# Optimization experiments

Measured on AMD Instinct MI355X. Metric: run time of the kernel, lower is better.

The kernel has to match this reference:

```python
import jax, jax.numpy as jnp
import numpy as np

N_NODES = 100000
N_EDGES = 1600000
IN_C, HID_C, OUT_C = 128, 128, 64


def setup_inputs() -> dict:
    key = jax.random.key(0)
    ks = jax.random.split(key, 6)
    x = jax.random.normal(ks[0], (N_NODES, IN_C), dtype=jnp.float32)
    edge_index = jax.random.randint(ks[1], (2, N_EDGES), 0, N_NODES)
    W1 = jax.random.normal(ks[2], (IN_C, HID_C), dtype=jnp.float32) * (1.0 / np.sqrt(IN_C))
    b1 = jnp.zeros((HID_C,), dtype=jnp.float32)
    W2 = jax.random.normal(ks[3], (HID_C, OUT_C), dtype=jnp.float32) * (1.0 / np.sqrt(HID_C))
    b2 = jnp.zeros((OUT_C,), dtype=jnp.float32)
    return {"x": x, "edge_index": edge_index, "W1": W1, "b1": b1, "W2": W2, "b2": b2}


def gcn_conv(x, W, b, src, dst):
    # PyG GCNConv: D^{-1/2} (A + I) D^{-1/2} X W + b, with self-loops handled
    # analytically (no explicit self-loop edges materialized).
    h = x @ W                                             # [N, d_out]
    ones = jnp.ones(src.shape[0], dtype=h.dtype)
    deg = jax.ops.segment_sum(ones, dst, num_segments=N_NODES) + 1.0  # +1 self-loop
    dinv = jax.lax.rsqrt(deg)                             # deg >= 1, safe
    norm = dinv[src] * dinv[dst]                          # [E]
    msg = h[src] * norm[:, None]                          # gather + scale  [E, d_out]
    agg = jax.ops.segment_sum(msg, dst, num_segments=N_NODES)
    agg = agg + h * (dinv * dinv)[:, None]                # self-loop contribution
    return agg + b


def reference(x, edge_index, W1, b1, W2, b2):
    src, dst = edge_index[0], edge_index[1]
    h = jax.nn.relu(gcn_conv(x, W1, b1, src, dst))
    # dropout is identity in eval mode
    out = gcn_conv(h, W2, b2, src, dst)
    return out
```

## Files before the change

### kernel.cpp

```cpp
#include <hip/hip_runtime.h>

#define N_NODESC 100000
#define N_EDGESC 1600000
#define NB_BUCKETS 391
#define BUCKET_CAP 5120
#define CHUNK_A 4096

typedef __attribute__((ext_vector_type(4))) float floatx4;
typedef __attribute__((ext_vector_type(8))) short shortx8;

__device__ __forceinline__ unsigned short f32_to_bf16_rne(float f) {
    unsigned int u = __float_as_uint(f);
    unsigned int r = u + 0x7fffu + ((u >> 16) & 1u);
    return (unsigned short)(r >> 16);
}
__device__ __forceinline__ float bf16_to_f32(unsigned short h) {
    return __uint_as_float(((unsigned int)h) << 16);
}
__device__ __forceinline__ float bflo(unsigned int u) { return __uint_as_float(u << 16); }
__device__ __forceinline__ float bfhi(unsigned int u) { return __uint_as_float(u & 0xffff0000u); }
__device__ __forceinline__ unsigned int pack2bf(float a, float b) {
    return ((unsigned int)f32_to_bf16_rne(b) << 16) | (unsigned int)f32_to_bf16_rne(a);
}

__global__ __launch_bounds__(256) void k_wfrag_all(const float* __restrict__ W1,
        const float* __restrict__ W2,
        unsigned short* __restrict__ w1hi, unsigned short* __restrict__ w1lo,
        unsigned short* __restrict__ w2hi, unsigned short* __restrict__ w2lo,
        int* __restrict__ gcur) {
    int t = threadIdx.x;
    if (blockIdx.x == 0)
        for (int i = t; i < NB_BUCKETS; i += 256) gcur[i] = i * BUCKET_CAP;
    int idx = blockIdx.x * 256 + t;
    float f;
    int k, col, C, o;
    unsigned short *phi, *plo;
    if (idx < 16384) {
        k = idx >> 7; col = idx & 127; C = 8;
        f = W1[idx]; phi = w1hi; plo = w1lo;
    } else {
        int idx2 = idx - 16384;
        k = idx2 >> 6; col = idx2 & 63; C = 4;
        f = W2[idx2]; phi = w2hi; plo = w2lo;
    }
    unsigned short hi = f32_to_bf16_rne(f);
    unsigned short lo = f32_to_bf16_rne(f - bf16_to_f32(hi));
    int kc = k >> 5, q = (k >> 3) & 3, j = k & 7;
    int c = col >> 4, n = col & 15;
    o = (((kc * C + c) * 4 + q) * 16 + n) * 8 + j;
    phi[o] = hi; plo[o] = lo;
}

__global__ __launch_bounds__(1024) void k_bucket(const int* __restrict__ src,
        const int* __restrict__ dst, int* __restrict__ gcur,
        unsigned int* __restrict__ tmp) {
    __shared__ int hist[NB_BUCKETS];
    int t = threadIdx.x;
    for (int i = t; i < NB_BUCKETS; i += 1024) hist[i] = 0;
    __syncthreads();
    int base = blockIdx.x * CHUNK_A;
    int end = min(base + CHUNK_A, N_EDGESC);
    for (int e = base + t; e < end; e += 1024)
        atomicAdd(&hist[dst[e] >> 8], 1);
    __syncthreads();
    for (int i = t; i < NB_BUCKETS; i += 1024) {
        int c = hist[i];
        hist[i] = (c > 0) ? atomicAdd(&gcur[i], c) : 0;
    }
    __syncthreads();
    for (int e = base + t; e < end; e += 1024) {
        int d = dst[e];
        int pos = atomicAdd(&hist[d >> 8], 1);
        tmp[pos] = ((unsigned int)src[e] << 8) | (unsigned int)(d & 255);
    }
}

__global__ __launch_bounds__(1024) void k_place(const unsigned int* __restrict__ tmp,
        const int* __restrict__ gcur,
        int* __restrict__ swsrc, int* __restrict__ deg,
        int* __restrict__ row_ptr, float* __restrict__ dinv) {
    __shared__ int hist[256], scan[256], lcur[256];
    int b = blockIdx.x, t = threadIdx.x;
    int start = b * BUCKET_CAP;
    int end = gcur[b];
    if (t < 256) hist[t] = 0;
    __syncthreads();
    for (int i = start + t; i < end; i += 1024)
        atomicAdd(&hist[tmp[i] & 255u], 1);
    __syncthreads();
    int own = (t < 256) ? hist[t] : 0;
    if (t < 256) scan[t] = own;
    __syncthreads();
    for (int off = 1; off < 256; off <<= 1) {
        int add = (t >= off && t < 256) ? scan[t - off] : 0;
        __syncthreads();
        if (t < 256) scan[t] += add;
        __syncthreads();
    }
    if (t < 256) {
        int rp = start + scan[t] - own;
        lcur[t] = rp;
        int node = (b << 8) + t;
        if (node < N_NODESC) {
            deg[node] = own;
            row_ptr[node] = rp;
            dinv[node] = rsqrtf((float)own + 1.0f);
        }
    }
    __syncthreads();
    for (int i = start + t; i < end; i += 1024) {
        unsigned int v = tmp[i];
        int pos = atomicAdd(&lcur[v & 255u], 1);
        swsrc[pos] = (int)(v >> 8);
    }
}

template<int NOUT, int AFP32>
__global__ __launch_bounds__(256) void k_gemm_mfma(const void* __restrict__ Xv,
        const unsigned short* __restrict__ whi, const unsigned short* __restrict__ wlo,
        const float* __restrict__ dinv, unsigned short* __restrict__ H) {
    constexpr int C = NOUT / 16;
    constexpr int PITCH = NOUT + 4;
    __shared__ __align__(16) float etile[4][16][PITCH];
    int wv = threadIdx.x >> 6, lane = threadIdx.x & 63;
    int n16 = lane & 15, q = lane >> 4;
    int rowBase = blockIdx.x * 128 + wv * 32;
    floatx4 acc[2][C];
#pragma unroll
    for (int m = 0; m < 2; ++m)
#pragma unroll
        for (int c = 0; c < C; ++c) acc[m][c] = (floatx4){0.f, 0.f, 0.f, 0.f};

    const shortx8* whi8 = (const shortx8*)whi;
    const shortx8* wlo8 = (const shortx8*)wlo;

    for (int kc = 0; kc < 4; ++kc) {
        shortx8 ahi[2], alo[2];
#pragma unroll
        for (int m = 0; m < 2; ++m) {
            int r = rowBase + m * 16 + n16;
            if (r >= N_NODESC) r = N_NODESC - 1;
            if (AFP32) {
                const float* xp = &((const float*)Xv)[(size_t)r * 128 + kc * 32 + q * 8];
                floatx4 x0 = *(const floatx4*)xp;
                floatx4 x1 = *(const floatx4*)(xp + 4);
#pragma unroll
                for (int jj = 0; jj < 4; ++jj) {
                    unsigned short h0 = f32_to_bf16_rne(x0[jj]);
                    ahi[m][jj] = (short)h0;
                    alo[m][jj] = (short)f32_to_bf16_rne(x0[jj] - bf16_to_f32(h0));
                    unsigned short h1 = f32_to_bf16_rne(x1[jj]);
                    ahi[m][jj + 4] = (short)h1;
                    alo[m][jj + 4] = (short)f32_to_bf16_rne(x1[jj] - bf16_to_f32(h1));
                }
            } else {
                const unsigned short* xp = &((const unsigned short*)Xv)[(size_t)r * 128 + kc * 32 + q * 8];
                ahi[m] = *(const shortx8*)xp;
            }
        }
#pragma unroll
        for (int c = 0; c < C; ++c) {
            int fo = (kc * C + c) * 64 + lane;
            shortx8 bhi = whi8[fo];
            shortx8 blo = wlo8[fo];
#pragma unroll
            for (int m = 0; m < 2; ++m) {
                acc[m][c] = __builtin_amdgcn_mfma_f32_16x16x32_bf16(ahi[m], bhi, acc[m][c], 0, 0, 0);
                if (AFP32)
                    acc[m][c] = __builtin_amdgcn_mfma_f32_16x16x32_bf16(alo[m], bhi, acc[m][c], 0, 0, 0);
                acc[m][c] = __builtin_amdgcn_mfma_f32_16x16x32_bf16(ahi[m], blo, acc[m][c], 0, 0, 0);
            }
        }
    }
    constexpr int CPL = NOUT / 4;
#pragma unroll
    for (int m = 0; m < 2; ++m) {
        __syncthreads();
#pragma unroll
        for (int c = 0; c < C; ++c)
#pragma unroll
            for (int reg = 0; reg < 4; ++reg)
                etile[wv][q * 4 + reg][c * 16 + n16] = acc[m][c][reg];
        __syncthreads();
        int row = lane >> 2, cb = lane & 3;
        int r = rowBase + m * 16 + row;
        if (r < N_NODESC) {
            float dv = dinv[r];
            unsigned int po[CPL / 2];
#pragma unroll
            for (int i = 0; i < CPL / 4; ++i) {
                floatx4 v = *(const floatx4*)&etile[wv][row][cb * CPL + i * 4];
                po[i * 2 + 0] = pack2bf(v[0] * dv, v[1] * dv);
                po[i * 2 + 1] = pack2bf(v[2] * dv, v[3] * dv);
            }
            unsigned int* op = (unsigned int*)&H[(size_t)r * NOUT + cb * CPL];
#pragma unroll
            for (int i = 0; i < CPL / 8; ++i)
                *(uint4*)(op + i * 4) = *(uint4*)&po[i * 4];
        }
    }
}

__global__ __launch_bounds__(256) void k_agg128(const unsigned short* __restrict__ Hb,
        const int* __restrict__ swsrc, const int* __restrict__ row_ptr,
        const int* __restrict__ deg, const float* __restrict__ dinv,
        const float* __restrict__ bias, unsigned short* __restrict__ outb) {
    int node = blockIdx.x * 4 + (threadIdx.x >> 6);
    int lane = threadIdx.x & 63;
    int g = lane >> 4, l16 = lane & 15;
    int start = row_ptr[node];
    int end = start + deg[node];
    float acc[8] = {0.f, 0.f, 0.f, 0.f, 0.f, 0.f, 0.f, 0.f};
    int j = start + g;
    for (; j + 4 < end; j += 8) {
        int s0 = swsrc[j];
        int s1 = swsrc[j + 4];
        uint4 v0 = *(const uint4*)(Hb + (size_t)s0 * 128 + l16 * 8);
        uint4 v1 = *(const uint4*)(Hb + (size_t)s1 * 128 + l16 * 8);
        acc[0] += bflo(v0.x) + bflo(v1.x);
        acc[1] += bfhi(v0.x) + bfhi(v1.x);
        acc[2] += bflo(v0.y) + bflo(v1.y);
        acc[3] += bfhi(v0.y) + bfhi(v1.y);
        acc[4] += bflo(v0.z) + bflo(v1.z);
        acc[5] += bfhi(v0.z) + bfhi(v1.z);
        acc[6] += bflo(v0.w) + bflo(v1.w);
        acc[7] += bfhi(v0.w) + bfhi(v1.w);
    }
    if (j < end) {
        int s0 = swsrc[j];
        uint4 v0 = *(const uint4*)(Hb + (size_t)s0 * 128 + l16 * 8);
        acc[0] += bflo(v0.x); acc[1] += bfhi(v0.x);
        acc[2] += bflo(v0.y); acc[3] += bfhi(v0.y);
        acc[4] += bflo(v0.z); acc[5] += bfhi(v0.z);
        acc[6] += bflo(v0.w); acc[7] += bfhi(v0.w);
    }
#pragma unroll
    for (int i = 0; i < 8; ++i) {
        acc[i] += __shfl_xor(acc[i], 16);
        acc[i] += __shfl_xor(acc[i], 32);
    }
    if (g == 0) {
        float dv = dinv[node];
        uint4 sv = *(const uint4*)(Hb + (size_t)node * 128 + l16 * 8);
        floatx4 b0 = *(const floatx4*)&bias[l16 * 8];
        floatx4 b1 = *(const floatx4*)&bias[l16 * 8 + 4];
        float o0 = dv * (acc[0] + bflo(sv.x)) + b0[0];
        float o1 = dv * (acc[1] + bfhi(sv.x)) + b0[1];
        float o2 = dv * (acc[2] + bflo(sv.y)) + b0[2];
        float o3 = dv * (acc[3] + bfhi(sv.y)) + b0[3];
        float o4 = dv * (acc[4] + bflo(sv.z)) + b1[0];
        float o5 = dv * (acc[5] + bfhi(sv.z)) + b1[1];
        float o6 = dv * (acc[6] + bflo(sv.w)) + b1[2];
        float o7 = dv * (acc[7] + bfhi(sv.w)) + b1[3];
        uint4 o;
        o.x = pack2bf(fmaxf(o0, 0.f), fmaxf(o1, 0.f));
        o.y = pack2bf(fmaxf(o2, 0.f), fmaxf(o3, 0.f));
        o.z = pack2bf(fmaxf(o4, 0.f), fmaxf(o5, 0.f));
        o.w = pack2bf(fmaxf(o6, 0.f), fmaxf(o7, 0.f));
        *(uint4*)(outb + (size_t)node * 128 + l16 * 8) = o;
    }
}

__global__ __launch_bounds__(256) void k_agg64(const unsigned short* __restrict__ Hb,
        const int* __restrict__ swsrc, const int* __restrict__ row_ptr,
        const int* __restrict__ deg, const float* __restrict__ dinv,
        const float* __restrict__ bias, float* __restrict__ out) {
    int node = blockIdx.x * 4 + (threadIdx.x >> 6);
    int lane = threadIdx.x & 63;
    int g = lane >> 3, l8 = lane & 7;
    int start = row_ptr[node];
    int end = start + deg[node];
    float acc[8] = {0.f, 0.f, 0.f, 0.f, 0.f, 0.f, 0.f, 0.f};
    int j = start + g;
    for (; j + 8 < end; j += 16) {
        int s0 = swsrc[j];
        int s1 = swsrc[j + 8];
        uint4 v0 = *(const uint4*)(Hb + (size_t)s0 * 64 + l8 * 8);
        uint4 v1 = *(const uint4*)(Hb + (size_t)s1 * 64 + l8 * 8);
        acc[0] += bflo(v0.x) + bflo(v1.x);
        acc[1] += bfhi(v0.x) + bfhi(v1.x);
        acc[2] += bflo(v0.y) + bflo(v1.y);
        acc[3] += bfhi(v0.y) + bfhi(v1.y);
        acc[4] += bflo(v0.z) + bflo(v1.z);
        acc[5] += bfhi(v0.z) + bfhi(v1.z);
        acc[6] += bflo(v0.w) + bflo(v1.w);
        acc[7] += bfhi(v0.w) + bfhi(v1.w);
    }
    if (j < end) {
        int s0 = swsrc[j];
        uint4 v0 = *(const uint4*)(Hb + (size_t)s0 * 64 + l8 * 8);
        acc[0] += bflo(v0.x); acc[1] += bfhi(v0.x);
        acc[2] += bflo(v0.y); acc[3] += bfhi(v0.y);
        acc[4] += bflo(v0.z); acc[5] += bfhi(v0.z);
        acc[6] += bflo(v0.w); acc[7] += bfhi(v0.w);
    }
#pragma unroll
    for (int i = 0; i < 8; ++i) {
        acc[i] += __shfl_xor(acc[i], 8);
        acc[i] += __shfl_xor(acc[i], 16);
        acc[i] += __shfl_xor(acc[i], 32);
    }
    if (g == 0) {
        float dv = dinv[node];
        uint4 sv = *(const uint4*)(Hb + (size_t)node * 64 + l8 * 8);
        floatx4 b0 = *(const floatx4*)&bias[l8 * 8];
        floatx4 b1 = *(const floatx4*)&bias[l8 * 8 + 4];
        floatx4 o0, o1;
        o0[0] = dv * (acc[0] + bflo(sv.x)) + b0[0];
        o0[1] = dv * (acc[1] + bfhi(sv.x)) + b0[1];
        o0[2] = dv * (acc[2] + bflo(sv.y)) + b0[2];
        o0[3] = dv * (acc[3] + bfhi(sv.y)) + b0[3];
        o1[0] = dv * (acc[4] + bflo(sv.z)) + b1[0];
        o1[1] = dv * (acc[5] + bfhi(sv.z)) + b1[1];
        o1[2] = dv * (acc[6] + bflo(sv.w)) + b1[2];
        o1[3] = dv * (acc[7] + bfhi(sv.w)) + b1[3];
        *(floatx4*)&out[(size_t)node * 64 + l8 * 8] = o0;
        *(floatx4*)&out[(size_t)node * 64 + l8 * 8 + 4] = o1;
    }
}

extern "C" void kernel_launch(void* const* d_in, const int* in_sizes, int n_in,
                              void* d_out, int out_size, void* d_ws, size_t ws_size,
                              hipStream_t stream) {
    const float* x  = (const float*)d_in[0];
    const int*   ei = (const int*)d_in[1];
    const float* W1 = (const float*)d_in[2];
    const float* b1 = (const float*)d_in[3];
    const float* W2 = (const float*)d_in[4];
    const float* b2 = (const float*)d_in[5];
    float* out = (float*)d_out;
    const int* src = ei;
    const int* dst = ei + N_EDGESC;

    char* ws = (char*)d_ws;
    size_t off = 0;
    auto alloc = [&](size_t bytes) -> void* {
        off = (off + 255) & ~(size_t)255;
        void* p = ws + off;
        off += bytes;
        return p;
    };
    const size_t CSR_SLOTS = (size_t)NB_BUCKETS * BUCKET_CAP;
    int*   deg     = (int*)  alloc((size_t)N_NODESC * 4);
    float* dinv    = (float*)alloc((size_t)N_NODESC * 4);
    int*   row_ptr = (int*)  alloc((size_t)N_NODESC * 4);
    int*   gcur    = (int*)  alloc(NB_BUCKETS * 4);
    unsigned int* tmp   = (unsigned int*)alloc(CSR_SLOTS * 4);
    int*   swsrc   = (int*)  alloc(CSR_SLOTS * 4);
    unsigned short* w1hi = (unsigned short*)alloc(128 * 128 * 2);
    unsigned short* w1lo = (unsigned short*)alloc(128 * 128 * 2);
    unsigned short* w2hi = (unsigned short*)alloc(128 * 64 * 2);
    unsigned short* w2lo = (unsigned short*)alloc(128 * 64 * 2);
    unsigned short* h1b  = (unsigned short*)alloc((size_t)N_NODESC * 128 * 2);
    unsigned short* hb   = (unsigned short*)alloc((size_t)N_NODESC * 128 * 2);
    unsigned short* h2b  = h1b;

    const int nbGemm = (N_NODESC + 127) / 128;
    const int nbBkt  = (N_EDGESC + CHUNK_A - 1) / CHUNK_A;

    k_wfrag_all<<<(16384 + 8192) / 256, 256, 0, stream>>>(W1, W2, w1hi, w1lo, w2hi, w2lo, gcur);
    k_bucket<<<nbBkt, 1024, 0, stream>>>(src, dst, gcur, tmp);
    k_place<<<NB_BUCKETS, 1024, 0, stream>>>(tmp, gcur, swsrc, deg, row_ptr, dinv);

    k_gemm_mfma<128, 1><<<nbGemm, 256, 0, stream>>>(x, w1hi, w1lo, dinv, h1b);
    k_agg128<<<N_NODESC / 4, 256, 0, stream>>>(h1b, swsrc, row_ptr, deg, dinv, b1, hb);
    k_gemm_mfma<64, 0><<<nbGemm, 256, 0, stream>>>(hb, w2hi, w2lo, dinv, h2b);
    k_agg64<<<N_NODESC / 4, 256, 0, stream>>>(h2b, swsrc, row_ptr, deg, dinv, b2, out);
}
```

Before: 281.8 us.

## Fuse layer-1 aggregation with layer-2 GEMM via LDS tile and MFMA

Layer-1 aggregation and the layer-2 linear transform now run in one kernel. Each 256-thread block aggregates 16 nodes into an XOR-swizzled LDS tile, then runs bf16 MFMA against the split W2 and writes the dinv-scaled H2 directly. This drops the round trip of the 128-wide hidden activation through global memory and removes one kernel launch. Separately, the remaining GEMM epilogue swaps its block-wide __syncthreads for wave barriers plus lgkmcnt waits, since each wave only touches its own LDS tile. The cost is less parallelism per node during gathering (four nodes per wave, processed in sequence) and scalar 2-byte output stores.

```diff
diff --git a/kernel.cpp b/kernel.cpp
--- a/kernel.cpp
+++ b/kernel.cpp
@@ -175,13 +175,14 @@
     constexpr int CPL = NOUT / 4;
 #pragma unroll
     for (int m = 0; m < 2; ++m) {
-        __syncthreads();
+        __builtin_amdgcn_wave_barrier();
 #pragma unroll
         for (int c = 0; c < C; ++c)
 #pragma unroll
             for (int reg = 0; reg < 4; ++reg)
                 etile[wv][q * 4 + reg][c * 16 + n16] = acc[m][c][reg];
-        __syncthreads();
+        asm volatile("s_waitcnt lgkmcnt(0)" ::: "memory");
+        __builtin_amdgcn_wave_barrier();
         int row = lane >> 2, cb = lane & 3;
         int r = rowBase + m * 16 + row;
         if (r < N_NODESC) {
@@ -198,66 +199,102 @@
             for (int i = 0; i < CPL / 8; ++i)
                 *(uint4*)(op + i * 4) = *(uint4*)&po[i * 4];
         }
-    }
-}
-
-__global__ __launch_bounds__(256) void k_agg128(const unsigned short* __restrict__ Hb,
+        asm volatile("s_waitcnt lgkmcnt(0)" ::: "memory");
+        __builtin_amdgcn_wave_barrier();
+    }
+}
+
+__global__ __launch_bounds__(256) void k_agg_gemm(const unsigned short* __restrict__ Hb,
         const int* __restrict__ swsrc, const int* __restrict__ row_ptr,
         const int* __restrict__ deg, const float* __restrict__ dinv,
-        const float* __restrict__ bias, unsigned short* __restrict__ outb) {
-    int node = blockIdx.x * 4 + (threadIdx.x >> 6);
-    int lane = threadIdx.x & 63;
+        const float* __restrict__ bias,
+        const unsigned short* __restrict__ w2hi, const unsigned short* __restrict__ w2lo,
+        unsigned short* __restrict__ H2) {
+    __shared__ __align__(16) unsigned int lds_h[16][64];
+    int wv = threadIdx.x >> 6, lane = threadIdx.x & 63;
     int g = lane >> 4, l16 = lane & 15;
-    int start = row_ptr[node];
-    int end = start + deg[node];
-    float acc[8] = {0.f, 0.f, 0.f, 0.f, 0.f, 0.f, 0.f, 0.f};
-    int j = start + g;
-    for (; j + 4 < end; j += 8) {
-        int s0 = swsrc[j];
-        int s1 = swsrc[j + 4];
-        uint4 v0 = *(const uint4*)(Hb + (size_t)s0 * 128 + l16 * 8);
-        uint4 v1 = *(const uint4*)(Hb + (size_t)s1 * 128 + l16 * 8);
-        acc[0] += bflo(v0.x) + bflo(v1.x);
-        acc[1] += bfhi(v0.x) + bfhi(v1.x);
-        acc[2] += bflo(v0.y) + bflo(v1.y);
-        acc[3] += bfhi(v0.y) + bfhi(v1.y);
-        acc[4] += bflo(v0.z) + bflo(v1.z);
-        acc[5] += bfhi(v0.z) + bfhi(v1.z);
-        acc[6] += bflo(v0.w) + bflo(v1.w);
-        acc[7] += bfhi(v0.w) + bfhi(v1.w);
-    }
-    if (j < end) {
-        int s0 = swsrc[j];
-        uint4 v0 = *(const uint4*)(Hb + (size_t)s0 * 128 + l16 * 8);
-        acc[0] += bflo(v0.x); acc[1] += bfhi(v0.x);
-        acc[2] += bflo(v0.y); acc[3] += bfhi(v0.y);
-        acc[4] += bflo(v0.z); acc[5] += bfhi(v0.z);
-        acc[6] += bflo(v0.w); acc[7] += bfhi(v0.w);
-    }
-#pragma unroll
-    for (int i = 0; i < 8; ++i) {
-        acc[i] += __shfl_xor(acc[i], 16);
-        acc[i] += __shfl_xor(acc[i], 32);
-    }
-    if (g == 0) {
-        float dv = dinv[node];
-        uint4 sv = *(const uint4*)(Hb + (size_t)node * 128 + l16 * 8);
-        floatx4 b0 = *(const floatx4*)&bias[l16 * 8];
-        floatx4 b1 = *(const floatx4*)&bias[l16 * 8 + 4];
-        float o0 = dv * (acc[0] + bflo(sv.x)) + b0[0];
-        float o1 = dv * (acc[1] + bfhi(sv.x)) + b0[1];
-        float o2 = dv * (acc[2] + bflo(sv.y)) + b0[2];
-        float o3 = dv * (acc[3] + bfhi(sv.y)) + b0[3];
-        float o4 = dv * (acc[4] + bflo(sv.z)) + b1[0];
-        float o5 = dv * (acc[5] + bfhi(sv.z)) + b1[1];
-        float o6 = dv * (acc[6] + bflo(sv.w)) + b1[2];
-        float o7 = dv * (acc[7] + bfhi(sv.w)) + b1[3];
-        uint4 o;
-        o.x = pack2bf(fmaxf(o0, 0.f), fmaxf(o1, 0.f));
-        o.y = pack2bf(fmaxf(o2, 0.f), fmaxf(o3, 0.f));
-        o.z = pack2bf(fmaxf(o4, 0.f), fmaxf(o5, 0.f));
-        o.w = pack2bf(fmaxf(o6, 0.f), fmaxf(o7, 0.f));
-        *(uint4*)(outb + (size_t)node * 128 + l16 * 8) = o;
+    int nb = blockIdx.x * 16;
+
+#pragma unroll
+    for (int i = 0; i < 4; ++i) {
+        int nt = wv * 4 + i;
+        int node = nb + nt;
+        int start = row_ptr[node];
+        int end = start + deg[node];
+        float acc[8] = {0.f, 0.f, 0.f, 0.f, 0.f, 0.f, 0.f, 0.f};
+        int j = start + g;
+        for (; j + 4 < end; j += 8) {
+            int s0 = swsrc[j];
+            int s1 = swsrc[j + 4];
+            uint4 v0 = *(const uint4*)(Hb + (size_t)s0 * 128 + l16 * 8);
+            uint4 v1 = *(const uint4*)(Hb + (size_t)s1 * 128 + l16 * 8);
+            acc[0] += bflo(v0.x) + bflo(v1.x);
+            acc[1] += bfhi(v0.x) + bfhi(v1.x);
+            acc[2] += bflo(v0.y) + bflo(v1.y);
+            acc[3] += bfhi(v0.y) + bfhi(v1.y);
+            acc[4] += bflo(v0.z) + bflo(v1.z);
+            acc[5] += bfhi(v0.z) + bfhi(v1.z);
+            acc[6] += bflo(v0.w) + bflo(v1.w);
+            acc[7] += bfhi(v0.w) + bfhi(v1.w);
+        }
+        if (j < end) {
+            int s0 = swsrc[j];
+            uint4 v0 = *(const uint4*)(Hb + (size_t)s0 * 128 + l16 * 8);
+            acc[0] += bflo(v0.x); acc[1] += bfhi(v0.x);
+            acc[2] += bflo(v0.y); acc[3] += bfhi(v0.y);
+            acc[4] += bflo(v0.z); acc[5] += bfhi(v0.z);
+            acc[6] += bflo(v0.w); acc[7] += bfhi(v0.w);
+        }
+#pragma unroll
+        for (int k = 0; k < 8; ++k) {
+            acc[k] += __shfl_xor(acc[k], 16);
+            acc[k] += __shfl_xor(acc[k], 32);
+        }
+        if (g == 0) {
+            float dv = dinv[node];
+            uint4 sv = *(const uint4*)(Hb + (size_t)node * 128 + l16 * 8);
+            floatx4 b0 = *(const floatx4*)&bias[l16 * 8];
+            floatx4 b1 = *(const floatx4*)&bias[l16 * 8 + 4];
+            float o0 = dv * (acc[0] + bflo(sv.x)) + b0[0];
+            float o1 = dv * (acc[1] + bfhi(sv.x)) + b0[1];
+            float o2 = dv * (acc[2] + bflo(sv.y)) + b0[2];
+            float o3 = dv * (acc[3] + bfhi(sv.y)) + b0[3];
+            float o4 = dv * (acc[4] + bflo(sv.z)) + b1[0];
+            float o5 = dv * (acc[5] + bfhi(sv.z)) + b1[1];
+            float o6 = dv * (acc[6] + bflo(sv.w)) + b1[2];
+            float o7 = dv * (acc[7] + bfhi(sv.w)) + b1[3];
+            uint4 o;
+            o.x = pack2bf(fmaxf(o0, 0.f), fmaxf(o1, 0.f));
+            o.y = pack2bf(fmaxf(o2, 0.f), fmaxf(o3, 0.f));
+            o.z = pack2bf(fmaxf(o4, 0.f), fmaxf(o5, 0.f));
+            o.w = pack2bf(fmaxf(o6, 0.f), fmaxf(o7, 0.f));
+            int pcol = (l16 * 4) ^ ((nt & 7) * 4);
+            *(uint4*)&lds_h[nt][pcol] = o;
+        }
+    }
+    __syncthreads();
+
+    int q = lane >> 4, n16 = lane & 15;
+    floatx4 accm = (floatx4){0.f, 0.f, 0.f, 0.f};
+    const shortx8* whi8 = (const shortx8*)w2hi;
+    const shortx8* wlo8 = (const shortx8*)w2lo;
+#pragma unroll
+    for (int kc = 0; kc < 4; ++kc) {
+        int pcol = (kc * 16 + q * 4) ^ ((n16 & 7) * 4);
+        shortx8 ahi = *(const shortx8*)&lds_h[n16][pcol];
+        int fo = (kc * 4 + wv) * 64 + lane;
+        shortx8 bhi = whi8[fo];
+        shortx8 blo = wlo8[fo];
+        accm = __builtin_amdgcn_mfma_f32_16x16x32_bf16(ahi, bhi, accm, 0, 0, 0);
+        accm = __builtin_amdgcn_mfma_f32_16x16x32_bf16(ahi, blo, accm, 0, 0, 0);
+    }
+    int crow = (lane >> 4) * 4;
+    int ccol = wv * 16 + n16;
+#pragma unroll
+    for (int reg = 0; reg < 4; ++reg) {
+        int r = nb + crow + reg;
+        float dv = dinv[r];
+        H2[(size_t)r * 64 + ccol] = f32_to_bf16_rne(accm[reg] * dv);
     }
 }
 
@@ -352,8 +389,7 @@
     unsigned short* w2hi = (unsigned short*)alloc(128 * 64 * 2);
     unsigned short* w2lo = (unsigned short*)alloc(128 * 64 * 2);
     unsigned short* h1b  = (unsigned short*)alloc((size_t)N_NODESC * 128 * 2);
-    unsigned short* hb   = (unsigned short*)alloc((size_t)N_NODESC * 128 * 2);
-    unsigned short* h2b  = h1b;
+    unsigned short* h2b  = (unsigned short*)alloc((size_t)N_NODESC * 128 * 2);
 
     const int nbGemm = (N_NODESC + 127) / 128;
     const int nbBkt  = (N_EDGESC + CHUNK_A - 1) / CHUNK_A;
@@ -363,7 +399,7 @@
     k_place<<<NB_BUCKETS, 1024, 0, stream>>>(tmp, gcur, swsrc, deg, row_ptr, dinv);
 
     k_gemm_mfma<128, 1><<<nbGemm, 256, 0, stream>>>(x, w1hi, w1lo, dinv, h1b);
-    k_agg128<<<N_NODESC / 4, 256, 0, stream>>>(h1b, swsrc, row_ptr, deg, dinv, b1, hb);
-    k_gemm_mfma<64, 0><<<nbGemm, 256, 0, stream>>>(hb, w2hi, w2lo, dinv, h2b);
+    k_agg_gemm<<<N_NODESC / 16, 256, 0, stream>>>(h1b, swsrc, row_ptr, deg, dinv, b1,
+                                                  w2hi, w2lo, h2b);
     k_agg64<<<N_NODESC / 4, 256, 0, stream>>>(h2b, swsrc, row_ptr, deg, dinv, b2, out);
 }
```

After: 278.0 us. Within noise of the previous version (-1.4%).
